# Optimization experiments

Measured on AMD Instinct MI355X. Metric: run time of the kernel, lower is better.

## Reference

```python
import jax, jax.numpy as jnp
import numpy as np

B, IN, X, OUT, Z = 4096, 1024, 2048, 512, 6
RES = [False, False, 1, False, 3, False]  # residual_in from init_kwargs
KEEP_P = 0.5  # y: Bernoulli keep-probability for connectivity mask


def _masked_normal(kw, km, shape):
    w = jax.random.normal(kw, shape, dtype=jnp.float32)
    m = jax.random.bernoulli(km, KEEP_P, shape).astype(jnp.float32)
    return w * m


def setup_inputs() -> dict:
    key = jax.random.key(0)
    ks = jax.random.split(key, 40)
    inp = {}
    inp['x'] = jax.random.normal(ks[0], (B, IN), dtype=jnp.float32)
    # weights stored as (in, out) == torch weight.T; mask baked in as in apply_connectivity()
    inp['W_in'] = _masked_normal(ks[1], ks[2], (IN, X))
    inp['b_in'] = jax.random.normal(ks[3], (X,), dtype=jnp.float32)
    hidden_in = [2 * X if RES[i] is not False else X for i in range(Z)]
    for i in range(Z):
        inp[f'Wh{i}'] = _masked_normal(ks[4 + 2 * i], ks[5 + 2 * i], (hidden_in[i], X))
    inp['bh'] = jax.random.normal(ks[20], (Z, X), dtype=jnp.float32)
    inp['W_out'] = _masked_normal(ks[21], ks[22], (X, OUT))
    inp['b_out'] = jax.random.normal(ks[23], (OUT,), dtype=jnp.float32)
    # per-column clip maxima: Poisson(rate=10) as in RandomActivation
    inp['mo_in'] = jax.random.poisson(ks[24], 10.0, (X,)).astype(jnp.float32)
    inp['mo_h'] = jax.random.poisson(ks[25], 10.0, (Z, X)).astype(jnp.float32)
    inp['mo_out'] = jax.random.poisson(ks[26], 10.0, (OUT,)).astype(jnp.float32)
    # per-column activation function ids in [0,5)
    inp['aid_in'] = jax.random.randint(ks[27], (X,), 0, 5, dtype=jnp.int32)
    inp['aid_h'] = jax.random.randint(ks[28], (Z, X), 0, 5, dtype=jnp.int32)
    inp['aid_out'] = jax.random.randint(ks[29], (OUT,), 0, 5, dtype=jnp.int32)
    return inp


def _rand_act(v, aid, mo):
    # fused per-column activation select (RandomActivation) + clip
    acts = [jax.nn.relu(v), jax.nn.sigmoid(v), jnp.tanh(v),
            jnp.where(v >= 0, v, 0.1 * v),  # LeakyReLU(0.1)
            jax.nn.selu(v)]
    out = jnp.select([aid == k for k in range(5)], acts, acts[0])
    return jnp.minimum(out, mo)


def reference(x, W_in, b_in, Wh0, Wh1, Wh2, Wh3, Wh4, Wh5, bh,
              W_out, b_out, mo_in, mo_h, mo_out, aid_in, aid_h, aid_out):
    Ws = [Wh0, Wh1, Wh2, Wh3, Wh4, Wh5]
    h = _rand_act(x @ W_in + b_in, aid_in, mo_in)
    outs = [h]  # temp_outputs
    for i in range(Z):
        if RES[i] is False:
            t = outs[i]
        else:
            t = jnp.concatenate([outs[i], outs[RES[i]]], axis=-1)
        outs.append(_rand_act(t @ Ws[i] + bh[i], aid_h[i], mo_h[i]))
    return _rand_act(outs[-1] @ W_out + b_out, aid_out, mo_out)
```

## Files before the change

kernel.cpp:

```cpp
#include <hip/hip_runtime.h>
#include <stdint.h>
#include <string.h>

#define BDIM   4096
#define INDIM  1024
#define XDIM   2048
#define OUTDIM 512
#define MCH    (BDIM / 16)

#define LO_SCALE 2048.0f
#define INV_LO_SCALE (1.0f / 2048.0f)

typedef _Float16 f16x8 __attribute__((ext_vector_type(8)));
typedef float f32x4 __attribute__((ext_vector_type(4)));
typedef unsigned short u16x8 __attribute__((ext_vector_type(8)));
typedef unsigned short u16x4 __attribute__((ext_vector_type(4)));

__device__ __forceinline__ unsigned short h2u(_Float16 h) {
  unsigned short u;
  memcpy(&u, &h, 2);
  return u;
}

__device__ __forceinline__ void split_h(float v, unsigned short& h,
                                        unsigned short& l) {
  _Float16 hh = (_Float16)v;
  float r = v - (float)hh;
  _Float16 ll = (_Float16)(r * LO_SCALE);
  h = h2u(hh);
  l = h2u(ll);
}

__device__ __forceinline__ void gld_lds16(const void* g, void* l) {
  __builtin_amdgcn_global_load_lds(
      (const __attribute__((address_space(1))) uint32_t*)g,
      (__attribute__((address_space(3))) uint32_t*)l, 16, 0, 0);
}

__device__ __forceinline__ float rand_act(float v, int a, float mo) {
  float r;
  if (a == 0) {
    r = fmaxf(v, 0.0f);
  } else if (a == 1) {
    r = 1.0f / (1.0f + expf(-v));
  } else if (a == 2) {
    r = tanhf(v);
  } else if (a == 3) {
    r = (v >= 0.0f) ? v : 0.1f * v;
  } else {
    r = (v > 0.0f) ? 1.0507009873554805f * v
                   : 1.7580993408473766f * expm1f(v);
  }
  return fminf(r, mo);
}


__global__ void pack_x(const float* __restrict__ s,
                       unsigned short* __restrict__ dh,
                       unsigned short* __restrict__ dl, int Kin) {
  int ks = blockIdx.x;
  int mblk = blockIdx.y;
  int cc = threadIdx.x >> 6;
  int lane = threadIdx.x & 63;
  int m16 = lane & 15, quad = lane >> 4;
  int row = mblk * 64 + cc * 16 + m16;
  const float* src = s + (size_t)row * Kin + ks * 32 + quad * 8;
  size_t o = ((size_t)ks * MCH + mblk * 4 + cc) * 512 + lane * 8;
  float4 v0 = *(const float4*)src;
  float4 v1 = *(const float4*)(src + 4);
  float vs[8] = {v0.x, v0.y, v0.z, v0.w, v1.x, v1.y, v1.z, v1.w};
  u16x8 vh, vl;
#pragma unroll
  for (int j = 0; j < 8; j++) {
    unsigned short h, l;
    split_h(vs[j], h, l);
    vh[j] = h;
    vl[j] = l;
  }
  *(u16x8*)(dh + o) = vh;
  *(u16x8*)(dl + o) = vl;
}

__global__ void pack_w(const float* __restrict__ W,
                       unsigned short* __restrict__ dh,
                       unsigned short* __restrict__ dl, int K, int N) {
  __shared__ float t[32][33];
  int n0 = blockIdx.x * 32, k0 = blockIdx.y * 32;
  int tx = threadIdx.x, ty = threadIdx.y;
#pragma unroll
  for (int i = 0; i < 32; i += 8)
    t[ty + i][tx] = W[(size_t)(k0 + ty + i) * N + n0 + tx];
  __syncthreads();
  int tt = ty * 32 + tx;
  int ci = tt >> 7;
  int rem = tt & 127;
  int lane = rem >> 1;
  int j4 = (rem & 1) * 4;
  int m16 = lane & 15, quad = lane >> 4;
  size_t o = ((size_t)(k0 >> 5) * (N >> 4) + (n0 >> 4) + ci) * 512 +
             lane * 8 + j4;
  u16x4 vh, vl;
#pragma unroll
  for (int jj = 0; jj < 4; jj++) {
    float v = t[quad * 8 + j4 + jj][ci * 16 + m16];
    unsigned short h, l;
    split_h(v, h, l);
    vh[jj] = h;
    vl[jj] = l;
  }
  *(u16x4*)(dh + o) = vh;
  *(u16x4*)(dl + o) = vl;
}

template <bool OUT_F16>
__global__ __launch_bounds__(256, 3) void gemm_split_act(
    const short* __restrict__ A1h, const short* __restrict__ A1l,
    const short* __restrict__ A2h, const short* __restrict__ A2l,
    const short* __restrict__ BTh, const short* __restrict__ BTl,
    const float* __restrict__ bias, const float* __restrict__ mo,
    const int* __restrict__ aid, unsigned short* __restrict__ Ch,
    unsigned short* __restrict__ Cl, float* __restrict__ Cf, int N, int K,
    int Ksplit) {
  __shared__ short lds0[8 * 512];
  __shared__ short lds1[8 * 512];
  __shared__ short lds2[8 * 512];

  const int tid = threadIdx.x;
  const int lane = tid & 63;
  const int wave = tid >> 6;
  const int m16 = lane & 15, quad = lane >> 4;

  const int blockN = blockIdx.x * 128;
  const int blockM = blockIdx.y * 64;

  f32x4 acc1[4][2];
  f32x4 acc2[4][2];
#pragma unroll
  for (int i = 0; i < 4; i++)
#pragma unroll
    for (int j = 0; j < 2; j++) {
      acc1[i][j] = (f32x4){0.f, 0.f, 0.f, 0.f};
      acc2[i][j] = (f32x4){0.f, 0.f, 0.f, 0.f};
    }

  const int KSTEPS = K >> 5;
  const int KS1 = Ksplit >> 5;

  const short* sAh = A1h;
  const short* sAl = A1l;
  const size_t aBase0 = (size_t)(blockM >> 4) * 512 + lane * 8;
  size_t aOff = aBase0;
  int stageK = 0;
  auto stageNext = [&](short* dst) {
#pragma unroll
    for (int s = 0; s < 2; s++) {
      int g = wave * 2 + s;
      const short* plane = (g < 4) ? sAh : sAl;
      gld_lds16(plane + aOff + (g & 3) * 512, dst + g * 512);
    }
    aOff += (size_t)MCH * 512;
    if (++stageK == KS1) { sAh = A2h; sAl = A2l; aOff = aBase0; }
  };

  size_t bOff = ((size_t)(blockN >> 4) + wave * 2) * 512 + lane * 8;
  const size_t bStride = (size_t)N * 32;
  auto loadBNext = [&](f16x8 (&bH)[2], f16x8 (&bL)[2]) {
    bH[0] = *(const f16x8*)(BTh + bOff);
    bH[1] = *(const f16x8*)(BTh + bOff + 512);
    bL[0] = *(const f16x8*)(BTl + bOff);
    bL[1] = *(const f16x8*)(BTl + bOff + 512);
    bOff += bStride;
  };

  f16x8 aH[4], aL[4];
  f16x8 b0H[2], b0L[2], b1H[2], b1L[2];

  auto ldsRead = [&](const short* src) {
#pragma unroll
    for (int t = 0; t < 4; t++)
      aH[t] = *(const f16x8*)&src[t * 512 + lane * 8];
#pragma unroll
    for (int t = 0; t < 4; t++)
      aL[t] = *(const f16x8*)&src[(4 + t) * 512 + lane * 8];
  };

  auto ph12 = [&](f16x8 (&bH)[2], f16x8 (&bL)[2]) {
    __builtin_amdgcn_s_setprio(1);
#pragma unroll
    for (int i = 0; i < 4; i++)
#pragma unroll
      for (int j = 0; j < 2; j++)
        acc1[i][j] = __builtin_amdgcn_mfma_f32_16x16x32_f16(aH[i], bH[j],
                                                            acc1[i][j], 0, 0, 0);
#pragma unroll
    for (int i = 0; i < 4; i++)
#pragma unroll
      for (int j = 0; j < 2; j++)
        acc2[i][j] = __builtin_amdgcn_mfma_f32_16x16x32_f16(aH[i], bL[j],
                                                            acc2[i][j], 0, 0, 0);
    __builtin_amdgcn_s_setprio(0);
  };
  auto ph3 = [&](f16x8 (&bH)[2]) {
    __builtin_amdgcn_s_setprio(1);
#pragma unroll
    for (int i = 0; i < 4; i++)
#pragma unroll
      for (int j = 0; j < 2; j++)
        acc2[i][j] = __builtin_amdgcn_mfma_f32_16x16x32_f16(aL[i], bH[j],
                                                            acc2[i][j], 0, 0, 0);
    __builtin_amdgcn_s_setprio(0);
  };

#define SB0 __builtin_amdgcn_sched_barrier(0)

  stageNext(lds0);
  loadBNext(b0H, b0L);
  stageNext(lds1);
  asm volatile("s_waitcnt vmcnt(6)" ::: "memory");
  __builtin_amdgcn_s_barrier();
  SB0;

  short *p0 = lds0, *p1 = lds1, *p2 = lds2;
  for (int ks = 0; ks <= KSTEPS - 4; ks += 2) {
    ldsRead(p0);
    loadBNext(b1H, b1L);
    stageNext(p2);
    SB0;
    asm volatile("s_waitcnt vmcnt(8)" ::: "memory");
    SB0;
    ph12(b0H, b0L);
    ph3(b0H);
    SB0;
    asm volatile("s_waitcnt vmcnt(6)" ::: "memory");
    __builtin_amdgcn_s_barrier();
    SB0;
    ldsRead(p1);
    loadBNext(b0H, b0L);
    stageNext(p0);
    SB0;
    asm volatile("s_waitcnt vmcnt(8)" ::: "memory");
    SB0;
    ph12(b1H, b1L);
    ph3(b1H);
    SB0;
    asm volatile("s_waitcnt vmcnt(6)" ::: "memory");
    __builtin_amdgcn_s_barrier();
    SB0;
    short* t = p0; p0 = p2; p2 = p1; p1 = t;
  }

  ldsRead(p0);
  loadBNext(b1H, b1L);
  SB0;
  asm volatile("s_waitcnt vmcnt(6)" ::: "memory");
  SB0;
  ph12(b0H, b0L);
  ph3(b0H);
  SB0;
  asm volatile("s_waitcnt vmcnt(4)" ::: "memory");
  __builtin_amdgcn_s_barrier();
  SB0;
  ldsRead(p1);
  SB0;
  asm volatile("s_waitcnt vmcnt(0)" ::: "memory");
  SB0;
  ph12(b1H, b1L);
  ph3(b1H);

#pragma unroll
  for (int j = 0; j < 2; j++) {
    int col = blockN + wave * 32 + j * 16 + m16;
    float b = bias[col];
    float m = mo[col];
    int a = aid[col];
    size_t kbase = OUT_F16 ? ((size_t)(col >> 5) * MCH) * 512 +
                                 (size_t)((col >> 3) & 3) * 128 + (col & 7)
                           : 0;
#pragma unroll
    for (int i = 0; i < 4; i++) {
#pragma unroll
      for (int r = 0; r < 4; r++) {
        int row = blockM + i * 16 + quad * 4 + r;
        float s = acc1[i][j][r] + acc2[i][j][r] * INV_LO_SCALE;
        float v = rand_act(s + b, a, m);
        if (OUT_F16) {
          unsigned short h, l;
          split_h(v, h, l);
          size_t pidx = kbase + (size_t)(row >> 4) * 512 + (row & 15) * 8;
          Ch[pidx] = h;
          Cl[pidx] = l;
        } else {
          Cf[(size_t)row * N + col] = v;
        }
      }
    }
  }
}

extern "C" void kernel_launch(void* const* d_in, const int* in_sizes, int n_in,
                              void* d_out, int out_size, void* d_ws,
                              size_t ws_size, hipStream_t stream) {
  (void)in_sizes; (void)n_in; (void)out_size; (void)ws_size;

  const float* x     = (const float*)d_in[0];
  const float* W_in  = (const float*)d_in[1];
  const float* b_in  = (const float*)d_in[2];
  const float* Wh[6] = {(const float*)d_in[3], (const float*)d_in[4],
                        (const float*)d_in[5], (const float*)d_in[6],
                        (const float*)d_in[7], (const float*)d_in[8]};
  const float* bh    = (const float*)d_in[9];
  const float* W_out = (const float*)d_in[10];
  const float* b_out = (const float*)d_in[11];
  const float* mo_in = (const float*)d_in[12];
  const float* mo_h  = (const float*)d_in[13];
  const float* mo_out= (const float*)d_in[14];
  const int* aid_in  = (const int*)d_in[15];
  const int* aid_h   = (const int*)d_in[16];
  const int* aid_out = (const int*)d_in[17];

  const int hin[6] = {XDIM, XDIM, 2 * XDIM, XDIM, 2 * XDIM, XDIM};

  char* p = (char*)d_ws;
  auto take = [&](size_t elems) {
    short* q = (short*)p;
    p += elems * 2 * 2;
    return q;
  };
  short* x_s = take((size_t)BDIM * INDIM);
  size_t xpl = (size_t)BDIM * INDIM;
  short* w_in_s = take((size_t)XDIM * INDIM);
  size_t wpl_in = (size_t)XDIM * INDIM;
  short* w_h_s[6];
  size_t wpl_h[6];
  for (int i = 0; i < 6; i++) {
    wpl_h[i] = (size_t)XDIM * hin[i];
    w_h_s[i] = take(wpl_h[i]);
  }
  short* w_out_s = take((size_t)OUTDIM * XDIM);
  size_t wpl_out = (size_t)OUTDIM * XDIM;
  const size_t apl = (size_t)BDIM * XDIM;
  short* actA = take(apl);
  short* actB = take(apl);
  short* actC = take(apl);

  pack_x<<<dim3(INDIM / 32, BDIM / 64), dim3(256), 0, stream>>>(
      x, (unsigned short*)x_s, (unsigned short*)(x_s + xpl), INDIM);
  pack_w<<<dim3(XDIM / 32, INDIM / 32), dim3(32, 8), 0, stream>>>(
      W_in, (unsigned short*)w_in_s, (unsigned short*)(w_in_s + wpl_in), INDIM,
      XDIM);
  for (int i = 0; i < 6; i++)
    pack_w<<<dim3(XDIM / 32, hin[i] / 32), dim3(32, 8), 0, stream>>>(
        Wh[i], (unsigned short*)w_h_s[i],
        (unsigned short*)(w_h_s[i] + wpl_h[i]), hin[i], XDIM);
  pack_w<<<dim3(OUTDIM / 32, XDIM / 32), dim3(32, 8), 0, stream>>>(
      W_out, (unsigned short*)w_out_s, (unsigned short*)(w_out_s + wpl_out),
      XDIM, OUTDIM);

  auto G = [&](const short* A1, size_t a1pl, const short* A2, size_t a2pl,
               const short* W, size_t wpl, const float* bi, const float* m,
               const int* a, short* Cb, float* Cf, int N, int K, int Ks) {
    dim3 grid(N / 128, BDIM / 64);
    const short* A2h = A2;
    const short* A2l = A2 ? A2 + a2pl : nullptr;
    if (Cb)
      gemm_split_act<true><<<grid, 256, 0, stream>>>(
          A1, A1 + a1pl, A2h, A2l, W, W + wpl, bi, m, a, (unsigned short*)Cb,
          (unsigned short*)(Cb + apl), nullptr, N, K, Ks);
    else
      gemm_split_act<false><<<grid, 256, 0, stream>>>(
          A1, A1 + a1pl, A2h, A2l, W, W + wpl, bi, m, a, nullptr, nullptr, Cf,
          N, K, Ks);
  };

  G(x_s, xpl, nullptr, 0, w_in_s, wpl_in, b_in, mo_in, aid_in, actA, nullptr,
    XDIM, INDIM, INDIM);
  G(actA, apl, nullptr, 0, w_h_s[0], wpl_h[0], bh + 0 * XDIM, mo_h + 0 * XDIM,
    aid_h + 0 * XDIM, actB, nullptr, XDIM, XDIM, XDIM);
  G(actB, apl, nullptr, 0, w_h_s[1], wpl_h[1], bh + 1 * XDIM, mo_h + 1 * XDIM,
    aid_h + 1 * XDIM, actC, nullptr, XDIM, XDIM, XDIM);
  G(actC, apl, actB, apl, w_h_s[2], wpl_h[2], bh + 2 * XDIM, mo_h + 2 * XDIM,
    aid_h + 2 * XDIM, actA, nullptr, XDIM, 2 * XDIM, XDIM);
  G(actA, apl, nullptr, 0, w_h_s[3], wpl_h[3], bh + 3 * XDIM, mo_h + 3 * XDIM,
    aid_h + 3 * XDIM, actB, nullptr, XDIM, XDIM, XDIM);
  G(actB, apl, actA, apl, w_h_s[4], wpl_h[4], bh + 4 * XDIM, mo_h + 4 * XDIM,
    aid_h + 4 * XDIM, actC, nullptr, XDIM, 2 * XDIM, XDIM);
  G(actC, apl, nullptr, 0, w_h_s[5], wpl_h[5], bh + 5 * XDIM, mo_h + 5 * XDIM,
    aid_h + 5 * XDIM, actB, nullptr, XDIM, XDIM, XDIM);
  G(actB, apl, nullptr, 0, w_out_s, wpl_out, b_out, mo_out, aid_out, nullptr,
    (float*)d_out, OUTDIM, XDIM, XDIM);
}
```

Baseline: 1.225 ms.

## Restructure GEMM pipeline to double-buffered 64-wide K windows with occupancy 4

Replaces the triple-buffered per-32-K LDS ring with two LDS buffers, each holding two K-steps, so there is one barrier per 64 K instead of per 32. A-fragment LDS reads are interleaved with MFMA phases to cut register pressure, and launch bounds move from 3 to 4 waves per SIMD. Offsets switch from size_t to unsigned arithmetic. This trades prefetch depth (now one window ahead) for fewer barriers and higher occupancy, at some risk of exposed load latency or register spills.

New measurement: 1.149 ms. 6.3% less time.

```diff
diff --git a/kernel.cpp b/kernel.cpp
--- a/kernel.cpp
+++ b/kernel.cpp
@@ -113,7 +113,7 @@
 }
 
 template <bool OUT_F16>
-__global__ __launch_bounds__(256, 3) void gemm_split_act(
+__global__ __launch_bounds__(256, 4) void gemm_split_act(
     const short* __restrict__ A1h, const short* __restrict__ A1l,
     const short* __restrict__ A2h, const short* __restrict__ A2l,
     const short* __restrict__ BTh, const short* __restrict__ BTl,
@@ -121,9 +121,8 @@
     const int* __restrict__ aid, unsigned short* __restrict__ Ch,
     unsigned short* __restrict__ Cl, float* __restrict__ Cf, int N, int K,
     int Ksplit) {
-  __shared__ short lds0[8 * 512];
-  __shared__ short lds1[8 * 512];
-  __shared__ short lds2[8 * 512];
+  __shared__ short lds0[2 * 8 * 512];
+  __shared__ short lds1[2 * 8 * 512];
 
   const int tid = threadIdx.x;
   const int lane = tid & 63;
@@ -144,26 +143,31 @@
     }
 
   const int KSTEPS = K >> 5;
-  const int KS1 = Ksplit >> 5;
+  const int W = KSTEPS >> 1;
+  const int KS1W = (Ksplit >> 5) >> 1;
 
   const short* sAh = A1h;
   const short* sAl = A1l;
-  const size_t aBase0 = (size_t)(blockM >> 4) * 512 + lane * 8;
-  size_t aOff = aBase0;
-  int stageK = 0;
+  const unsigned aBase0 = (unsigned)((blockM >> 4) * 512 + lane * 8);
+  unsigned aOff = aBase0;
+  int stageW = 0;
   auto stageNext = [&](short* dst) {
 #pragma unroll
-    for (int s = 0; s < 2; s++) {
-      int g = wave * 2 + s;
-      const short* plane = (g < 4) ? sAh : sAl;
-      gld_lds16(plane + aOff + (g & 3) * 512, dst + g * 512);
+    for (int sub = 0; sub < 2; sub++) {
+#pragma unroll
+      for (int s = 0; s < 2; s++) {
+        int g = wave * 2 + s;
+        const short* plane = (g < 4) ? sAh : sAl;
+        gld_lds16(plane + aOff + sub * (MCH * 512) + (g & 3) * 512,
+                  dst + sub * 4096 + g * 512);
+      }
     }
-    aOff += (size_t)MCH * 512;
-    if (++stageK == KS1) { sAh = A2h; sAl = A2l; aOff = aBase0; }
-  };
-
-  size_t bOff = ((size_t)(blockN >> 4) + wave * 2) * 512 + lane * 8;
-  const size_t bStride = (size_t)N * 32;
+    aOff += 2u * (MCH * 512);
+    if (++stageW == KS1W) { sAh = A2h; sAl = A2l; aOff = aBase0; }
+  };
+
+  unsigned bOff = (unsigned)(((blockN >> 4) + wave * 2) * 512 + lane * 8);
+  const unsigned bStride = (unsigned)N * 32;
   auto loadBNext = [&](f16x8 (&bH)[2], f16x8 (&bL)[2]) {
     bH[0] = *(const f16x8*)(BTh + bOff);
     bH[1] = *(const f16x8*)(BTh + bOff + 512);
@@ -172,19 +176,14 @@
     bOff += bStride;
   };
 
-  f16x8 aH[4], aL[4];
   f16x8 b0H[2], b0L[2], b1H[2], b1L[2];
 
-  auto ldsRead = [&](const short* src) {
+  auto computeSub = [&](const short* buf, int sub, f16x8 (&bH)[2],
+                        f16x8 (&bL)[2]) {
+    f16x8 aH[4];
 #pragma unroll
     for (int t = 0; t < 4; t++)
-      aH[t] = *(const f16x8*)&src[t * 512 + lane * 8];
-#pragma unroll
-    for (int t = 0; t < 4; t++)
-      aL[t] = *(const f16x8*)&src[(4 + t) * 512 + lane * 8];
-  };
-
-  auto ph12 = [&](f16x8 (&bH)[2], f16x8 (&bL)[2]) {
+      aH[t] = *(const f16x8*)&buf[sub * 4096 + t * 512 + lane * 8];
     __builtin_amdgcn_s_setprio(1);
 #pragma unroll
     for (int i = 0; i < 4; i++)
@@ -199,8 +198,10 @@
         acc2[i][j] = __builtin_amdgcn_mfma_f32_16x16x32_f16(aH[i], bL[j],
                                                             acc2[i][j], 0, 0, 0);
     __builtin_amdgcn_s_setprio(0);
-  };
-  auto ph3 = [&](f16x8 (&bH)[2]) {
+    f16x8 aL[4];
+#pragma unroll
+    for (int t = 0; t < 4; t++)
+      aL[t] = *(const f16x8*)&buf[sub * 4096 + (4 + t) * 512 + lane * 8];
     __builtin_amdgcn_s_setprio(1);
 #pragma unroll
     for (int i = 0; i < 4; i++)
@@ -215,57 +216,29 @@
 
   stageNext(lds0);
   loadBNext(b0H, b0L);
-  stageNext(lds1);
-  asm volatile("s_waitcnt vmcnt(6)" ::: "memory");
-  __builtin_amdgcn_s_barrier();
-  SB0;
-
-  short *p0 = lds0, *p1 = lds1, *p2 = lds2;
-  for (int ks = 0; ks <= KSTEPS - 4; ks += 2) {
-    ldsRead(p0);
-    loadBNext(b1H, b1L);
-    stageNext(p2);
-    SB0;
-    asm volatile("s_waitcnt vmcnt(8)" ::: "memory");
-    SB0;
-    ph12(b0H, b0L);
-    ph3(b0H);
-    SB0;
-    asm volatile("s_waitcnt vmcnt(6)" ::: "memory");
-    __builtin_amdgcn_s_barrier();
-    SB0;
-    ldsRead(p1);
-    loadBNext(b0H, b0L);
-    stageNext(p0);
-    SB0;
-    asm volatile("s_waitcnt vmcnt(8)" ::: "memory");
-    SB0;
-    ph12(b1H, b1L);
-    ph3(b1H);
-    SB0;
-    asm volatile("s_waitcnt vmcnt(6)" ::: "memory");
-    __builtin_amdgcn_s_barrier();
-    SB0;
-    short* t = p0; p0 = p2; p2 = p1; p1 = t;
-  }
-
-  ldsRead(p0);
-  loadBNext(b1H, b1L);
-  SB0;
-  asm volatile("s_waitcnt vmcnt(6)" ::: "memory");
-  SB0;
-  ph12(b0H, b0L);
-  ph3(b0H);
-  SB0;
   asm volatile("s_waitcnt vmcnt(4)" ::: "memory");
   __builtin_amdgcn_s_barrier();
   SB0;
-  ldsRead(p1);
-  SB0;
-  asm volatile("s_waitcnt vmcnt(0)" ::: "memory");
-  SB0;
-  ph12(b1H, b1L);
-  ph3(b1H);
+
+  short* cur = lds0;
+  short* oth = lds1;
+  for (int w = 0; w < W - 1; ++w) {
+    loadBNext(b1H, b1L);
+    stageNext(oth);
+    computeSub(cur, 0, b0H, b0L);
+    SB0;
+    loadBNext(b0H, b0L);
+    computeSub(cur, 1, b1H, b1L);
+    SB0;
+    asm volatile("s_waitcnt vmcnt(4)" ::: "memory");
+    __builtin_amdgcn_s_barrier();
+    SB0;
+    short* t = cur; cur = oth; oth = t;
+  }
+
+  loadBNext(b1H, b1L);
+  computeSub(cur, 0, b0H, b0L);
+  computeSub(cur, 1, b1H, b1L);
 
 #pragma unroll
   for (int j = 0; j < 2; j++) {
```
